# Kernel tuning notes

Hardware: AMD Instinct MI355X
Metric: run time of the kernel (lower is better)

The kernel has to match this reference:

```python
import jax, jax.numpy as jnp
import numpy as np

N = 50000      # nodes
E = 400000     # edges
HID = 128      # hidden size
H = 8          # heads
HS = HID // H  # head size = 16
TN = 8         # node types
R = 8          # relation (edge) types
L = 2          # layers
OUT = 128
EPS = 1e-5
SQRT_D = float(np.sqrt(HS))


def setup_inputs() -> dict:
    key = jax.random.key(0)
    ks = jax.random.split(key, 12)
    s = 1.0 / np.sqrt(HID)
    sh = 1.0 / np.sqrt(HS)
    return {
        "x": jax.random.normal(ks[0], (N, HID), jnp.float32),
        "edge_index": jax.random.randint(ks[1], (2, E), 0, N, dtype=jnp.int32),
        "ntype": jax.random.randint(ks[2], (N,), 0, TN, dtype=jnp.int32),
        "etype": jax.random.randint(ks[3], (E,), 0, R, dtype=jnp.int32),
        "Wk": jax.random.normal(ks[4], (L, TN, HID, HID), jnp.float32) * s,
        "Wq": jax.random.normal(ks[5], (L, TN, HID, HID), jnp.float32) * s,
        "Wv": jax.random.normal(ks[6], (L, TN, HID, HID), jnp.float32) * s,
        "Wa": jax.random.normal(ks[7], (L, TN, HID, HID), jnp.float32) * s,
        "pri": jnp.ones((L, H, R), jnp.float32),
        "Watt": jax.random.normal(ks[8], (L, H, R, HS, HS), jnp.float32) * sh,
        "Wmsg": jax.random.normal(ks[9], (L, H, R, HS, HS), jnp.float32) * sh,
        "skip": jnp.ones((L, TN), jnp.float32),
        "ln_g": jnp.ones((L, HID), jnp.float32),
        "ln_b": jnp.zeros((L, HID), jnp.float32),
        "Wff": jax.random.normal(ks[10], (HID, OUT), jnp.float32) * s,
        "bff": jnp.zeros((OUT,), jnp.float32),
    }


def typed_linear(x, types, W):
    """x:(M,din), types:(M,), W:(T,din,dout) -> (M,dout); y = x @ W[type]."""
    out = jnp.zeros((x.shape[0], W.shape[-1]), x.dtype)
    for t in range(W.shape[0]):
        out = out + jnp.where((types == t)[:, None], x @ W[t], 0.0)
    return out


def rel_apply(h, etype, W):
    """h:(E,H,hs), etype:(E,), W:(H,R,hs,hs) -> (E,H,hs); per-head, per-relation linear."""
    out = jnp.zeros_like(h)
    for r in range(W.shape[1]):
        out = out + jnp.where((etype == r)[:, None, None],
                              jnp.einsum('ehi,hio->eho', h, W[:, r]), 0.0)
    return out


def gt_layer(x, src, dst, ntype, etype, Wk, Wq, Wv, Wa, pri, Watt, Wmsg, skip, g, b):
    n = x.shape[0]
    k = typed_linear(x, ntype, Wk).reshape(n, H, HS)
    q = typed_linear(x, ntype, Wq).reshape(n, H, HS)
    v = typed_linear(x, ntype, Wv).reshape(n, H, HS)
    k_j, q_i, v_j = k[src], q[dst], v[src]          # (E,H,hs)
    kw = rel_apply(k_j, etype, Watt)                # relation-specific key transform
    a = (kw * q_i).sum(-1) * pri[:, etype].T / SQRT_D  # (E,H)
    # scatter softmax over destination nodes
    amax = jax.ops.segment_max(a, dst, num_segments=n)
    ex = jnp.exp(a - amax[dst])
    den = jax.ops.segment_sum(ex, dst, num_segments=n)
    alpha = ex / (den[dst] + 1e-16)
    m = rel_apply(v_j, etype, Wmsg)                 # relation-specific message
    agg = jax.ops.segment_sum(alpha[..., None] * m, dst, num_segments=n)
    out = jax.nn.silu(typed_linear(agg.reshape(n, HID), ntype, Wa))
    al = jax.nn.sigmoid(skip[ntype])[:, None]
    out = out * al + x * (1.0 - al)                 # gated residual (in==hid)
    mu = out.mean(-1, keepdims=True)
    var = ((out - mu) ** 2).mean(-1, keepdims=True)
    return (out - mu) / jnp.sqrt(var + EPS) * g + b


def reference(x, edge_index, ntype, etype, Wk, Wq, Wv, Wa, pri, Watt, Wmsg,
              skip, ln_g, ln_b, Wff, bff):
    src, dst = edge_index[0], edge_index[1]
    emb = x
    for l in range(L):
        emb = gt_layer(emb, src, dst, ntype, etype, Wk[l], Wq[l], Wv[l], Wa[l],
                       pri[l], Watt[l], Wmsg[l], skip[l], ln_g[l], ln_b[l])
    return emb @ Wff + bff
```

## Files before the change

### kernel.cpp

```cpp
#include <hip/hip_runtime.h>
#include <hip/hip_bf16.h>
#include <math.h>

#define N_NODES 50000
#define N_EDGES 400000
#define HID 128
#define NH 8
#define HS 16
#define TN 8
#define NR 8
#define TILE 32
#define MAXTILES 1571
#define PERM_SZ (MAXTILES * TILE)
#define SCAN_BLKS ((N_NODES + 255) / 256)
#define RL_CAP 400128
#define T_GRID 3280

typedef __attribute__((ext_vector_type(8))) short bf16x8;
typedef __attribute__((ext_vector_type(4))) float f32x4;

__device__ __forceinline__ unsigned short f2bf(float f) {
    __hip_bfloat16 h = __float2bfloat16(f);
    return *reinterpret_cast<unsigned short*>(&h);
}
__device__ __forceinline__ float bf2f(unsigned short u) {
    return __uint_as_float((unsigned)u << 16);
}

__global__ void hist_kernel(const int* __restrict__ ntype, int* __restrict__ cnt) {
    __shared__ int l[TN];
    if (threadIdx.x < TN) l[threadIdx.x] = 0;
    __syncthreads();
    int i = blockIdx.x * 256 + threadIdx.x;
    if (i < N_NODES) atomicAdd(&l[ntype[i]], 1);
    __syncthreads();
    if (threadIdx.x < TN) atomicAdd(&cnt[threadIdx.x], l[threadIdx.x]);
}
__global__ void scan_kernel(const int* __restrict__ cnt, int* __restrict__ cursor) {
    if (threadIdx.x == 0 && blockIdx.x == 0) {
        int acc = 0;
        for (int t = 0; t < TN; ++t) {
            cursor[t] = acc;
            acc += ((cnt[t] + TILE - 1) / TILE) * TILE;
        }
    }
}
__global__ void scatter_kernel(const int* __restrict__ ntype, int* __restrict__ cursor,
                               int* __restrict__ perm) {
    __shared__ int lcnt[TN], lbase[TN];
    if (threadIdx.x < TN) lcnt[threadIdx.x] = 0;
    __syncthreads();
    int i = blockIdx.x * 256 + threadIdx.x;
    int t = 0, off = 0;
    if (i < N_NODES) {
        t = ntype[i];
        off = atomicAdd(&lcnt[t], 1);
    }
    __syncthreads();
    if (threadIdx.x < TN)
        lbase[threadIdx.x] = atomicAdd(&cursor[threadIdx.x], lcnt[threadIdx.x]);
    __syncthreads();
    if (i < N_NODES) perm[lbase[t] + off] = i;
}

__global__ void hist_dst_kernel(const int* __restrict__ dst, int* __restrict__ cnt) {
    int e = blockIdx.x * 256 + threadIdx.x;
    if (e < N_EDGES) atomicAdd(&cnt[dst[e]], 1);
}
__global__ void scan_block_kernel(const int* __restrict__ cnt, int* __restrict__ excl,
                                  int* __restrict__ bsum) {
    __shared__ int s[256];
    int tid = threadIdx.x;
    int i = blockIdx.x * 256 + tid;
    int v = (i < N_NODES) ? cnt[i] : 0;
    s[tid] = v;
    __syncthreads();
    for (int off = 1; off < 256; off <<= 1) {
        int t = (tid >= off) ? s[tid - off] : 0;
        __syncthreads();
        s[tid] += t;
        __syncthreads();
    }
    if (i < N_NODES) excl[i] = s[tid] - v;
    if (tid == 255) bsum[blockIdx.x] = s[255];
}
__global__ void scan_top_kernel(int* __restrict__ bsum) {
    __shared__ int s[256];
    int tid = threadIdx.x;
    int v = (tid < SCAN_BLKS) ? bsum[tid] : 0;
    s[tid] = v;
    __syncthreads();
    for (int off = 1; off < 256; off <<= 1) {
        int t = (tid >= off) ? s[tid - off] : 0;
        __syncthreads();
        s[tid] += t;
        __syncthreads();
    }
    if (tid < SCAN_BLKS) bsum[tid] = s[tid] - v;
}
__global__ void scan_add_kernel(int* __restrict__ excl, const int* __restrict__ bsum,
                                int* __restrict__ cursor) {
    int i = blockIdx.x * 256 + threadIdx.x;
    if (i < N_NODES) {
        int v = excl[i] + bsum[blockIdx.x];
        excl[i] = v;
        cursor[i] = v;
    }
}
__global__ void csr_scatter_kernel(const int* __restrict__ src, const int* __restrict__ dst,
                                   const int* __restrict__ etype, int* __restrict__ cur_dst,
                                   int* __restrict__ csr_sd, int* __restrict__ csr_et) {
    int e = blockIdx.x * 256 + threadIdx.x;
    if (e < N_EDGES) {
        int p = atomicAdd(&cur_dst[dst[e]], 1);
        csr_sd[p] = src[e] | (dst[e] << 16);
        csr_et[p] = etype[e];
    }
}

__global__ void ehist_kernel(const int* __restrict__ etype, int* __restrict__ ecnt) {
    __shared__ int l[NR];
    if (threadIdx.x < NR) l[threadIdx.x] = 0;
    __syncthreads();
    int e = blockIdx.x * 256 + threadIdx.x;
    if (e < N_EDGES) atomicAdd(&l[etype[e]], 1);
    __syncthreads();
    if (threadIdx.x < NR) atomicAdd(&ecnt[threadIdx.x], l[threadIdx.x]);
}
__global__ void escan_kernel(const int* __restrict__ ecnt, int* __restrict__ rbase,
                             int* __restrict__ rcur) {
    if (threadIdx.x == 0 && blockIdx.x == 0) {
        int acc = 0;
        for (int r = 0; r < NR; ++r) {
            rbase[r] = acc; rcur[r] = acc;
            acc += ((ecnt[r] + 15) / 16) * 16;
        }
        rbase[NR] = acc;
    }
}
__global__ void rinit_kernel(int* __restrict__ rsd, int* __restrict__ rpos) {
    int i = blockIdx.x * 256 + threadIdx.x;
    if (i < RL_CAP) { rsd[i] = 0; rpos[i] = N_EDGES; }
}
__global__ void rel_scatter_kernel(const int* __restrict__ csr_sd, const int* __restrict__ csr_et,
                                   int* __restrict__ rcur, int* __restrict__ rsd,
                                   int* __restrict__ rpos) {
    __shared__ int lcnt[NR], lbase[NR];
    if (threadIdx.x < NR) lcnt[threadIdx.x] = 0;
    __syncthreads();
    int p = blockIdx.x * 256 + threadIdx.x;
    int r = 0, off = 0;
    if (p < N_EDGES) {
        r = csr_et[p];
        off = atomicAdd(&lcnt[r], 1);
    }
    __syncthreads();
    if (threadIdx.x < NR) lbase[threadIdx.x] = atomicAdd(&rcur[threadIdx.x], lcnt[threadIdx.x]);
    __syncthreads();
    if (p < N_EDGES) {
        int rp = lbase[r] + off;
        rsd[rp] = csr_sd[p];
        rpos[rp] = p;
    }
}

__global__ void wconv_kernel(const float* __restrict__ W, unsigned short* __restrict__ out) {
    int mat = blockIdx.x >> 3, seg = blockIdx.x & 7;
    const float* w = W + (size_t)mat * HID * HID;
    unsigned short* o = out + (size_t)mat * HID * HID;
#pragma unroll
    for (int c = 0; c < 8; ++c) {
        int idx = seg * 2048 + c * 256 + threadIdx.x;
        int i = idx >> 7, j = idx & 127;
        o[j * HID + i] = f2bf(w[idx]);
    }
}
__global__ void wsmall_conv(const float* __restrict__ W, const float* __restrict__ pri,
                            unsigned short* __restrict__ out) {
    int blk = blockIdx.x;
    int tid = threadIdx.x;
    int i = tid >> 4, o = tid & 15;
    float s = pri ? pri[blk] * 0.25f : 1.f;
    out[blk * 256 + o * 16 + i] = f2bf(W[blk * 256 + i * 16 + o] * s);
}

__global__ __launch_bounds__(256) void gemm3_mfma(
    const float* __restrict__ x, const int* __restrict__ perm, const int* __restrict__ ntype,
    const unsigned short* __restrict__ WkT, const unsigned short* __restrict__ WqT,
    const unsigned short* __restrict__ WvT,
    unsigned short* __restrict__ Kb, unsigned short* __restrict__ Qb,
    unsigned short* __restrict__ Vb) {
    __shared__ unsigned short xs[TILE][HID + 8];
    __shared__ int nodes[TILE];
    int tid = threadIdx.x;
    if (tid < TILE) nodes[tid] = perm[blockIdx.x * TILE + tid];
    __syncthreads();
    if (nodes[0] < 0) return;
    int t = ntype[nodes[0]];
#pragma unroll
    for (int c = 0; c < 4; ++c) {
        int v = tid + c * 256;
        int ns = v >> 5, ii = (v & 31) * 4;
        int node = nodes[ns];
        float4 val = (node >= 0) ? *(const float4*)(x + (size_t)node * HID + ii)
                                 : make_float4(0.f, 0.f, 0.f, 0.f);
        uint2 pk;
        pk.x = (unsigned)f2bf(val.x) | ((unsigned)f2bf(val.y) << 16);
        pk.y = (unsigned)f2bf(val.z) | ((unsigned)f2bf(val.w) << 16);
        *(uint2*)&xs[ns][ii] = pk;
    }
    __syncthreads();
    int wv = tid >> 6, lane = tid & 63;
    int lrow = lane & 15, lk = lane >> 4;
    bf16x8 af[2][4];
#pragma unroll
    for (int rt = 0; rt < 2; ++rt)
#pragma unroll
        for (int kk = 0; kk < 4; ++kk)
            af[rt][kk] = *(const bf16x8*)&xs[rt * 16 + lrow][kk * 32 + lk * 8];
    size_t woff = (size_t)t * HID * HID + (size_t)lrow * HID + lk * 8;
#pragma unroll
    for (int pp = 0; pp < 6; ++pp) {
        int p = wv * 6 + pp;
        int mat = p >> 3, ct = p & 7;
        const unsigned short* wb =
            (mat == 0 ? WkT : (mat == 1 ? WqT : WvT)) + woff + (size_t)ct * 16 * HID;
        unsigned short* ob = (mat == 0) ? Kb : (mat == 1 ? Qb : Vb);
        f32x4 a0 = {0.f, 0.f, 0.f, 0.f}, a1 = {0.f, 0.f, 0.f, 0.f};
#pragma unroll
        for (int kk = 0; kk < 4; ++kk) {
            bf16x8 bfr = *(const bf16x8*)(wb + kk * 32);
            a0 = __builtin_amdgcn_mfma_f32_16x16x32_bf16(af[0][kk], bfr, a0, 0, 0, 0);
            a1 = __builtin_amdgcn_mfma_f32_16x16x32_bf16(af[1][kk], bfr, a1, 0, 0, 0);
        }
        int col = ct * 16 + lrow;
#pragma unroll
        for (int q = 0; q < 4; ++q) {
            int r0 = lk * 4 + q;
            int n0 = nodes[r0], n1 = nodes[16 + r0];
            if (n0 >= 0) ob[(size_t)n0 * HID + col] = f2bf(a0[q]);
            if (n1 >= 0) ob[(size_t)n1 * HID + col] = f2bf(a1[q]);
        }
    }
}

__global__ __launch_bounds__(256) void gemm1_mfma(
    const float* __restrict__ x, const int* __restrict__ perm, const int* __restrict__ ntype,
    const unsigned short* __restrict__ Wt, const float* __restrict__ bias,
    float* __restrict__ out) {
    __shared__ unsigned short xs[TILE][HID + 8];
    __shared__ int nodes[TILE];
    int tid = threadIdx.x;
    if (tid < TILE) {
        int n;
        if (perm) n = perm[blockIdx.x * TILE + tid];
        else { n = blockIdx.x * TILE + tid; if (n >= N_NODES) n = -1; }
        nodes[tid] = n;
    }
    __syncthreads();
    if (nodes[0] < 0) return;
    int t = perm ? ntype[nodes[0]] : 0;
#pragma unroll
    for (int c = 0; c < 4; ++c) {
        int v = tid + c * 256;
        int ns = v >> 5, ii = (v & 31) * 4;
        int node = nodes[ns];
        float4 val = (node >= 0) ? *(const float4*)(x + (size_t)node * HID + ii)
                                 : make_float4(0.f, 0.f, 0.f, 0.f);
        uint2 pk;
        pk.x = (unsigned)f2bf(val.x) | ((unsigned)f2bf(val.y) << 16);
        pk.y = (unsigned)f2bf(val.z) | ((unsigned)f2bf(val.w) << 16);
        *(uint2*)&xs[ns][ii] = pk;
    }
    __syncthreads();
    int wv = tid >> 6, lane = tid & 63;
    int lrow = lane & 15, lk = lane >> 4;
    bf16x8 af[2][4];
#pragma unroll
    for (int rt = 0; rt < 2; ++rt)
#pragma unroll
        for (int kk = 0; kk < 4; ++kk)
            af[rt][kk] = *(const bf16x8*)&xs[rt * 16 + lrow][kk * 32 + lk * 8];
    const unsigned short* wb0 = Wt + (size_t)t * HID * HID + (size_t)lrow * HID + lk * 8;
#pragma unroll
    for (int pp = 0; pp < 2; ++pp) {
        int ct = wv * 2 + pp;
        const unsigned short* wb = wb0 + (size_t)ct * 16 * HID;
        f32x4 a0 = {0.f, 0.f, 0.f, 0.f}, a1 = {0.f, 0.f, 0.f, 0.f};
#pragma unroll
        for (int kk = 0; kk < 4; ++kk) {
            bf16x8 bfr = *(const bf16x8*)(wb + kk * 32);
            a0 = __builtin_amdgcn_mfma_f32_16x16x32_bf16(af[0][kk], bfr, a0, 0, 0, 0);
            a1 = __builtin_amdgcn_mfma_f32_16x16x32_bf16(af[1][kk], bfr, a1, 0, 0, 0);
        }
        float bv = bias ? bias[ct * 16 + lrow] : 0.f;
#pragma unroll
        for (int q = 0; q < 4; ++q) {
            int r0 = lk * 4 + q;
            int n0 = nodes[r0], n1 = nodes[16 + r0];
            if (n0 >= 0) out[(size_t)n0 * HID + ct * 16 + lrow] = a0[q] + bv;
            if (n1 >= 0) out[(size_t)n1 * HID + ct * 16 + lrow] = a1[q] + bv;
        }
    }
}

__global__ __launch_bounds__(256) void gemm1_ln_mfma(
    const unsigned short* __restrict__ aggb, const int* __restrict__ perm,
    const int* __restrict__ ntype, const unsigned short* __restrict__ Wt,
    const float* __restrict__ xin, const float* __restrict__ skip,
    const float* __restrict__ g, const float* __restrict__ b, float* __restrict__ xout) {
    __shared__ unsigned short xs[TILE][HID + 8];
    __shared__ int nodes[TILE];
    __shared__ float psum[TILE][4], psq[TILE][4];
    __shared__ float mu_s[TILE], rv_s[TILE];
    int tid = threadIdx.x;
    if (tid < TILE) nodes[tid] = perm[blockIdx.x * TILE + tid];
    __syncthreads();
    if (nodes[0] < 0) return;
    int t = ntype[nodes[0]];
#pragma unroll
    for (int c = 0; c < 4; ++c) {
        int v = tid + c * 256;
        int ns = v >> 5, ii = (v & 31) * 4;
        int node = nodes[ns];
        uint2 pk = make_uint2(0u, 0u);
        if (node >= 0) pk = *(const uint2*)(aggb + (size_t)node * HID + ii);
        *(uint2*)&xs[ns][ii] = pk;
    }
    __syncthreads();
    int wv = tid >> 6, lane = tid & 63;
    int lrow = lane & 15, lk = lane >> 4;
    bf16x8 af[2][4];
#pragma unroll
    for (int rt = 0; rt < 2; ++rt)
#pragma unroll
        for (int kk = 0; kk < 4; ++kk)
            af[rt][kk] = *(const bf16x8*)&xs[rt * 16 + lrow][kk * 32 + lk * 8];
    const unsigned short* wb0 = Wt + (size_t)t * HID * HID + (size_t)lrow * HID + lk * 8;
    float al = 1.f / (1.f + __expf(-skip[t]));
    float om = 1.f - al;
    float ov[2][2][4];
#pragma unroll
    for (int pp = 0; pp < 2; ++pp) {
        int ct = wv * 2 + pp;
        const unsigned short* wb = wb0 + (size_t)ct * 16 * HID;
        f32x4 a0 = {0.f, 0.f, 0.f, 0.f}, a1 = {0.f, 0.f, 0.f, 0.f};
#pragma unroll
        for (int kk = 0; kk < 4; ++kk) {
            bf16x8 bfr = *(const bf16x8*)(wb + kk * 32);
            a0 = __builtin_amdgcn_mfma_f32_16x16x32_bf16(af[0][kk], bfr, a0, 0, 0, 0);
            a1 = __builtin_amdgcn_mfma_f32_16x16x32_bf16(af[1][kk], bfr, a1, 0, 0, 0);
        }
        int col = ct * 16 + lrow;
#pragma unroll
        for (int q = 0; q < 4; ++q) {
            int n0 = nodes[lk * 4 + q], n1 = nodes[16 + lk * 4 + q];
            float s0 = a0[q] / (1.f + __expf(-a0[q]));
            float s1 = a1[q] / (1.f + __expf(-a1[q]));
            float x0 = (n0 >= 0) ? xin[(size_t)n0 * HID + col] : 0.f;
            float x1 = (n1 >= 0) ? xin[(size_t)n1 * HID + col] : 0.f;
            ov[pp][0][q] = s0 * al + x0 * om;
            ov[pp][1][q] = s1 * al + x1 * om;
        }
    }
#pragma unroll
    for (int half = 0; half < 2; ++half)
#pragma unroll
        for (int q = 0; q < 4; ++q) {
            float s = ov[0][half][q] + ov[1][half][q];
            float s2 = ov[0][half][q] * ov[0][half][q] + ov[1][half][q] * ov[1][half][q];
            s += __shfl_xor(s, 1); s += __shfl_xor(s, 2);
            s += __shfl_xor(s, 4); s += __shfl_xor(s, 8);
            s2 += __shfl_xor(s2, 1); s2 += __shfl_xor(s2, 2);
            s2 += __shfl_xor(s2, 4); s2 += __shfl_xor(s2, 8);
            if (lrow == 0) {
                int nd = half * 16 + lk * 4 + q;
                psum[nd][wv] = s;
                psq[nd][wv] = s2;
            }
        }
    __syncthreads();
    if (tid < TILE) {
        float s = psum[tid][0] + psum[tid][1] + psum[tid][2] + psum[tid][3];
        float s2 = psq[tid][0] + psq[tid][1] + psq[tid][2] + psq[tid][3];
        float mu = s * (1.f / HID);
        float var = s2 * (1.f / HID) - mu * mu;
        mu_s[tid] = mu;
        rv_s[tid] = rsqrtf(fmaxf(var, 0.f) + 1e-5f);
    }
    __syncthreads();
#pragma unroll
    for (int pp = 0; pp < 2; ++pp) {
        int col = (wv * 2 + pp) * 16 + lrow;
        float gg = g[col], bb = b[col];
#pragma unroll
        for (int q = 0; q < 4; ++q) {
            int i0 = lk * 4 + q, i1 = 16 + lk * 4 + q;
            int n0 = nodes[i0], n1 = nodes[i1];
            if (n0 >= 0) xout[(size_t)n0 * HID + col] = (ov[pp][0][q] - mu_s[i0]) * rv_s[i0] * gg + bb;
            if (n1 >= 0) xout[(size_t)n1 * HID + col] = (ov[pp][1][q] - mu_s[i1]) * rv_s[i1] * gg + bb;
        }
    }
}

__global__ __launch_bounds__(512) void transform_kernel(
    const unsigned short* __restrict__ Kb, const unsigned short* __restrict__ Vb,
    const unsigned short* __restrict__ Qb,
    const int* __restrict__ rsd, const int* __restrict__ rpos, const int* __restrict__ rbase,
    const unsigned short* __restrict__ WattT, const unsigned short* __restrict__ WmsgT,
    float* __restrict__ scores, unsigned short* __restrict__ mg) {
    __shared__ unsigned short smg[8][16][136];
    __shared__ float ssc[8][16][8];
    int wv = threadIdx.x >> 6;
    int r = wv;
    int lane = threadIdx.x & 63;
    int ecol = lane & 15, lk = lane >> 4;
    int tbeg = rbase[r] + blockIdx.x * 16;
    if (tbeg >= rbase[r + 1]) return;
    int entry = tbeg + ecol;
    int sd = rsd[entry];
    int s = sd & 0xFFFF, dd = (sd >> 16) & 0xFFFF;
    int p = rpos[entry];

    const bf16x8 zz = {0, 0, 0, 0, 0, 0, 0, 0};
#pragma unroll
    for (int h = 0; h < NH; ++h) {
        bf16x8 bk = zz, bv = zz, aa = zz, am = zz;
        if (lk < 2) {
            bk = *(const bf16x8*)(Kb + (size_t)s * HID + h * HS + lk * 8);
            bv = *(const bf16x8*)(Vb + (size_t)s * HID + h * HS + lk * 8);
            int wo = ((h * NR + r) * 16 + ecol) * 16 + lk * 8;
            aa = *(const bf16x8*)(WattT + wo);
            am = *(const bf16x8*)(WmsgT + wo);
        }
        f32x4 ck = {0.f, 0.f, 0.f, 0.f}, cm = {0.f, 0.f, 0.f, 0.f};
        ck = __builtin_amdgcn_mfma_f32_16x16x32_bf16(aa, bk, ck, 0, 0, 0);
        cm = __builtin_amdgcn_mfma_f32_16x16x32_bf16(am, bv, cm, 0, 0, 0);
        uint2 qraw = *(const uint2*)(Qb + (size_t)dd * HID + h * HS + lk * 4);
        float q0 = __uint_as_float(qraw.x << 16);
        float q1 = __uint_as_float(qraw.x & 0xffff0000u);
        float q2 = __uint_as_float(qraw.y << 16);
        float q3 = __uint_as_float(qraw.y & 0xffff0000u);
        float xsc = ck[0] * q0 + ck[1] * q1 + ck[2] * q2 + ck[3] * q3;
        xsc += __shfl_xor(xsc, 16);
        xsc += __shfl_xor(xsc, 32);
        if (lk == 0) ssc[wv][ecol][h] = xsc;
        uint2 pk2;
        pk2.x = (unsigned)f2bf(cm[0]) | ((unsigned)f2bf(cm[1]) << 16);
        pk2.y = (unsigned)f2bf(cm[2]) | ((unsigned)f2bf(cm[3]) << 16);
        *(uint2*)&smg[wv][ecol][h * 16 + lk * 4] = pk2;
    }
    int gq = lane >> 3, sub = lane & 7;
#pragma unroll
    for (int c = 0; c < 4; ++c) {
        int li = c * 8 + gq;
        int e = li >> 1, half = li & 1;
        int pe = __shfl(p, e);
        uint4 v = *(const uint4*)&smg[wv][e][half * 64 + sub * 8];
        *(uint4*)(mg + (size_t)pe * HID + half * 64 + sub * 8) = v;
    }
    int es = lane >> 1;
    int pe2 = __shfl(p, es & 15);
    if (lane < 32) {
        int hh = lane & 1;
        float4 v = *(const float4*)&ssc[wv][es][hh * 4];
        *(float4*)(scores + (size_t)pe2 * NH + hh * 4) = v;
    }
}

__global__ __launch_bounds__(256) void edge_soft_kernel(
    const float* __restrict__ scores, const unsigned short* __restrict__ mg,
    const int* __restrict__ row_ptr, const int* __restrict__ deg,
    unsigned short* __restrict__ aggb) {
    int d = blockIdx.x * 4 + (threadIdx.x >> 6);
    if (d >= N_NODES) return;
    int lane = threadIdx.x & 63;
    int h = lane >> 3, j = lane & 7;
    int beg = row_ptr[d], dg = deg[d];

    const float* sc = scores + (size_t)beg * NH + h;
    const unsigned short* mgp = mg + (size_t)beg * HID + h * HS + j * 2;

    float m = -INFINITY, den = 0.f, a0 = 0.f, a1 = 0.f;
    for (int e = 0; e < dg; ++e) {
        float a = sc[(size_t)e * NH];
        unsigned mgu = *(const unsigned*)(mgp + (size_t)e * HID);
        float g0 = __uint_as_float(mgu << 16);
        float g1 = __uint_as_float(mgu & 0xffff0000u);
        float mn = fmaxf(m, a);
        float scale = __expf(m - mn);
        float ex = __expf(a - mn);
        den = den * scale + ex;
        a0 = a0 * scale + ex * g0;
        a1 = a1 * scale + ex * g1;
        m = mn;
    }
    float inv = 1.f / (den + 1e-16f);
    unsigned r0 = (unsigned)f2bf(a0 * inv);
    unsigned r1 = (unsigned)f2bf(a1 * inv);
    *(unsigned*)(aggb + (size_t)d * HID + h * HS + j * 2) = r0 | (r1 << 16);
}

extern "C" void kernel_launch(void* const* d_in, const int* in_sizes, int n_in,
                              void* d_out, int out_size, void* d_ws, size_t ws_size,
                              hipStream_t stream) {
    const float* x     = (const float*)d_in[0];
    const int*   eidx  = (const int*)d_in[1];
    const int*   ntype = (const int*)d_in[2];
    const int*   etype = (const int*)d_in[3];
    const float* Wk    = (const float*)d_in[4];
    const float* Wq    = (const float*)d_in[5];
    const float* Wv    = (const float*)d_in[6];
    const float* Wa    = (const float*)d_in[7];
    const float* pri   = (const float*)d_in[8];
    const float* Watt  = (const float*)d_in[9];
    const float* Wmsg  = (const float*)d_in[10];
    const float* skip  = (const float*)d_in[11];
    const float* ln_g  = (const float*)d_in[12];
    const float* ln_b  = (const float*)d_in[13];
    const float* Wff   = (const float*)d_in[14];
    const float* bff   = (const float*)d_in[15];
    const int* src = eidx;
    const int* dst = eidx + N_EDGES;

    char* ws = (char*)d_ws;
    size_t szN = (size_t)N_NODES * HID * sizeof(float);
    float* embA = (float*)(ws);
    unsigned short* AGGb = (unsigned short*)(ws + szN);
    char*  kvq  = ws + 2 * szN;
    unsigned short* Kbf = (unsigned short*)kvq;
    unsigned short* Vbf = (unsigned short*)(kvq + (size_t)N_NODES * HID * 2);
    unsigned short* Qbf = (unsigned short*)(kvq + 2 * (size_t)N_NODES * HID * 2);
    float* l1out = (float*)kvq;
    char*  p    = kvq + 3 * (size_t)N_NODES * HID * 2;
    int* perm    = (int*)p;  p += (size_t)PERM_SZ * 4;
    int* cnt     = (int*)p;  p += TN * 4;
    int* cursor  = (int*)p;  p += TN * 4;
    int* row_ptr = (int*)p;  p += (size_t)N_NODES * 4;
    int* cnt_dst = (int*)p;  p += (size_t)N_NODES * 4;
    int* cur_dst = (int*)p;  p += (size_t)N_NODES * 4;
    int* bsum    = (int*)p;  p += 256 * 4;
    int* ecnt    = (int*)p;  p += NR * 4;
    int* rbase   = (int*)p;  p += (NR + 1) * 4;
    int* rcur    = (int*)p;  p += NR * 4;
    int* csr_sd  = (int*)p;  p += (size_t)N_EDGES * 4;
    int* csr_et  = (int*)p;  p += (size_t)N_EDGES * 4;
    int* rsd     = (int*)p;  p += (size_t)RL_CAP * 4;
    int* rpos    = (int*)p;  p += (size_t)RL_CAP * 4;
    size_t wmat = (size_t)HID * HID;
    unsigned short* WkT  = (unsigned short*)p;  p += 2 * TN * wmat * 2;
    unsigned short* WqT  = (unsigned short*)p;  p += 2 * TN * wmat * 2;
    unsigned short* WvT  = (unsigned short*)p;  p += 2 * TN * wmat * 2;
    unsigned short* WaT  = (unsigned short*)p;  p += 2 * TN * wmat * 2;
    unsigned short* WffT = (unsigned short*)p;  p += wmat * 2;
    unsigned short* WattT = (unsigned short*)p; p += 2 * 64 * 256 * 2;
    unsigned short* WmsgT = (unsigned short*)p; p += 2 * 64 * 256 * 2;
    p = (char*)(((size_t)p + 255) & ~(size_t)255);
    float* scores = (float*)p;          p += (size_t)(N_EDGES + 16) * NH * 4;
    unsigned short* mg = (unsigned short*)p;  p += (size_t)(N_EDGES + 16) * HID * 2;

    wconv_kernel<<<2 * TN * 8, 256, 0, stream>>>(Wk, WkT);
    wconv_kernel<<<2 * TN * 8, 256, 0, stream>>>(Wq, WqT);
    wconv_kernel<<<2 * TN * 8, 256, 0, stream>>>(Wv, WvT);
    wconv_kernel<<<2 * TN * 8, 256, 0, stream>>>(Wa, WaT);
    wconv_kernel<<<8, 256, 0, stream>>>(Wff, WffT);
    wsmall_conv<<<128, 256, 0, stream>>>(Watt, pri, WattT);
    wsmall_conv<<<128, 256, 0, stream>>>(Wmsg, nullptr, WmsgT);

    hipMemsetAsync(cnt, 0, TN * 4, stream);
    hipMemsetAsync(perm, 0xFF, (size_t)PERM_SZ * 4, stream);
    hist_kernel<<<(N_NODES + 255) / 256, 256, 0, stream>>>(ntype, cnt);
    scan_kernel<<<1, 64, 0, stream>>>(cnt, cursor);
    scatter_kernel<<<(N_NODES + 255) / 256, 256, 0, stream>>>(ntype, cursor, perm);

    hipMemsetAsync(cnt_dst, 0, (size_t)N_NODES * 4, stream);
    hipMemsetAsync(ecnt, 0, NR * 4, stream);
    hist_dst_kernel<<<(N_EDGES + 255) / 256, 256, 0, stream>>>(dst, cnt_dst);
    ehist_kernel<<<(N_EDGES + 255) / 256, 256, 0, stream>>>(etype, ecnt);
    scan_block_kernel<<<SCAN_BLKS, 256, 0, stream>>>(cnt_dst, row_ptr, bsum);
    scan_top_kernel<<<1, 256, 0, stream>>>(bsum);
    scan_add_kernel<<<SCAN_BLKS, 256, 0, stream>>>(row_ptr, bsum, cur_dst);
    csr_scatter_kernel<<<(N_EDGES + 255) / 256, 256, 0, stream>>>(src, dst, etype, cur_dst,
                                                                  csr_sd, csr_et);
    escan_kernel<<<1, 64, 0, stream>>>(ecnt, rbase, rcur);
    rinit_kernel<<<(RL_CAP + 255) / 256, 256, 0, stream>>>(rsd, rpos);
    rel_scatter_kernel<<<(N_EDGES + 255) / 256, 256, 0, stream>>>(csr_sd, csr_et, rcur,
                                                                  rsd, rpos);

    for (int l = 0; l < 2; ++l) {
        const float* xin = l ? embA : x;
        float* xout = l ? l1out : embA;
        const float* skip_l = skip + (size_t)l * TN;
        const float* g_l    = ln_g + (size_t)l * HID;
        const float* b_l    = ln_b + (size_t)l * HID;
        const unsigned short* WkT_l = WkT + (size_t)l * TN * wmat;
        const unsigned short* WqT_l = WqT + (size_t)l * TN * wmat;
        const unsigned short* WvT_l = WvT + (size_t)l * TN * wmat;
        const unsigned short* WaT_l = WaT + (size_t)l * TN * wmat;
        const unsigned short* WattT_l = WattT + (size_t)l * 64 * 256;
        const unsigned short* WmsgT_l = WmsgT + (size_t)l * 64 * 256;

        gemm3_mfma<<<MAXTILES, 256, 0, stream>>>(xin, perm, ntype, WkT_l, WqT_l, WvT_l,
                                                 Kbf, Qbf, Vbf);
        transform_kernel<<<T_GRID, 512, 0, stream>>>(Kbf, Vbf, Qbf, rsd, rpos, rbase,
                                                     WattT_l, WmsgT_l, scores, mg);
        edge_soft_kernel<<<(N_NODES + 3) / 4, 256, 0, stream>>>(scores, mg, row_ptr, cnt_dst,
                                                                AGGb);
        gemm1_ln_mfma<<<MAXTILES, 256, 0, stream>>>(AGGb, perm, ntype, WaT_l, xin,
                                                    skip_l, g_l, b_l, xout);
    }
    gemm1_mfma<<<(N_NODES + TILE - 1) / TILE, 256, 0, stream>>>(l1out, nullptr, ntype, WffT,
                                                                bff, (float*)d_out);
}
```

Before: 488.4 us.

## Fuse relation transform and segment softmax per destination-node block in LDS

Replaces the global relation-sorted edge lists with per-block relation tiles covering 16 destination nodes, built by a new btile_build kernel. A single fused kernel computes the relation-specific attention scores and messages with MFMA into shared memory, then does the online softmax aggregation directly from LDS. This removes the global round-trip of the per-edge scores and bf16 messages and one kernel launch per layer. In exchange it pads each relation to whole 16-edge tiles per block, which wastes some MFMA work, and it runs the heads in two passes. It also relies on fixed caps (288 edges and 26 tiles per block) that hold for these random inputs but are not guaranteed for arbitrary graphs.

```diff
diff --git a/kernel.cpp b/kernel.cpp
--- a/kernel.cpp
+++ b/kernel.cpp
@@ -13,8 +13,9 @@
 #define MAXTILES 1571
 #define PERM_SZ (MAXTILES * TILE)
 #define SCAN_BLKS ((N_NODES + 255) / 256)
-#define RL_CAP 400128
-#define T_GRID 3280
+#define NB 3125
+#define TPBMAX 26
+#define CAP 288
 
 typedef __attribute__((ext_vector_type(8))) short bf16x8;
 typedef __attribute__((ext_vector_type(4))) float f32x4;
@@ -118,49 +119,43 @@
     }
 }
 
-__global__ void ehist_kernel(const int* __restrict__ etype, int* __restrict__ ecnt) {
-    __shared__ int l[NR];
-    if (threadIdx.x < NR) l[threadIdx.x] = 0;
-    __syncthreads();
-    int e = blockIdx.x * 256 + threadIdx.x;
-    if (e < N_EDGES) atomicAdd(&l[etype[e]], 1);
-    __syncthreads();
-    if (threadIdx.x < NR) atomicAdd(&ecnt[threadIdx.x], l[threadIdx.x]);
-}
-__global__ void escan_kernel(const int* __restrict__ ecnt, int* __restrict__ rbase,
-                             int* __restrict__ rcur) {
-    if (threadIdx.x == 0 && blockIdx.x == 0) {
-        int acc = 0;
-        for (int r = 0; r < NR; ++r) {
-            rbase[r] = acc; rcur[r] = acc;
-            acc += ((ecnt[r] + 15) / 16) * 16;
-        }
-        rbase[NR] = acc;
-    }
-}
-__global__ void rinit_kernel(int* __restrict__ rsd, int* __restrict__ rpos) {
-    int i = blockIdx.x * 256 + threadIdx.x;
-    if (i < RL_CAP) { rsd[i] = 0; rpos[i] = N_EDGES; }
-}
-__global__ void rel_scatter_kernel(const int* __restrict__ csr_sd, const int* __restrict__ csr_et,
-                                   int* __restrict__ rcur, int* __restrict__ rsd,
-                                   int* __restrict__ rpos) {
-    __shared__ int lcnt[NR], lbase[NR];
-    if (threadIdx.x < NR) lcnt[threadIdx.x] = 0;
-    __syncthreads();
-    int p = blockIdx.x * 256 + threadIdx.x;
-    int r = 0, off = 0;
-    if (p < N_EDGES) {
-        r = csr_et[p];
-        off = atomicAdd(&lcnt[r], 1);
-    }
-    __syncthreads();
-    if (threadIdx.x < NR) lbase[threadIdx.x] = atomicAdd(&rcur[threadIdx.x], lcnt[threadIdx.x]);
-    __syncthreads();
-    if (p < N_EDGES) {
-        int rp = lbase[r] + off;
-        rsd[rp] = csr_sd[p];
-        rpos[rp] = p;
+__global__ void btile_build(const int* __restrict__ row_ptr,
+                            const int* __restrict__ csr_sd, const int* __restrict__ csr_et,
+                            int* __restrict__ btile_sd, int* __restrict__ btile_lp,
+                            int* __restrict__ btile_r, int* __restrict__ ntb) {
+    int b = blockIdx.x;
+    int lane = threadIdx.x;
+    int p0 = row_ptr[b * 16];
+    int p1 = (b == NB - 1) ? N_EDGES : row_ptr[b * 16 + 16];
+    int cnt = 0;
+    if (lane < 8) {
+        for (int p = p0; p < p1; ++p) cnt += (csr_et[p] == lane);
+    }
+    int tiles = (cnt + 15) >> 4;
+    int pre = 0, total = 0;
+    for (int k = 0; k < 8; ++k) {
+        int tk = __shfl(tiles, k);
+        if (k < lane) pre += tk;
+        total += tk;
+    }
+    if (lane == 0) ntb[b] = total;
+    if (lane < 8) {
+        int tbase = b * TPBMAX + pre;
+        for (int t = 0; t < tiles; ++t) btile_r[tbase + t] = lane;
+        int off = 0;
+        for (int p = p0; p < p1; ++p) {
+            if (csr_et[p] == lane) {
+                int idx = (tbase + (off >> 4)) * 16 + (off & 15);
+                btile_sd[idx] = csr_sd[p];
+                btile_lp[idx] = p - p0;
+                ++off;
+            }
+        }
+        for (; off < tiles * 16; ++off) {
+            int idx = (tbase + (off >> 4)) * 16 + (off & 15);
+            btile_sd[idx] = 0;
+            btile_lp[idx] = CAP;
+        }
     }
 }
 
@@ -403,102 +398,84 @@
     }
 }
 
-__global__ __launch_bounds__(512) void transform_kernel(
+__global__ __launch_bounds__(512) void fused_attn_kernel(
     const unsigned short* __restrict__ Kb, const unsigned short* __restrict__ Vb,
     const unsigned short* __restrict__ Qb,
-    const int* __restrict__ rsd, const int* __restrict__ rpos, const int* __restrict__ rbase,
+    const int* __restrict__ row_ptr, const int* __restrict__ deg,
+    const int* __restrict__ btile_sd, const int* __restrict__ btile_lp,
+    const int* __restrict__ btile_r, const int* __restrict__ ntb,
     const unsigned short* __restrict__ WattT, const unsigned short* __restrict__ WmsgT,
-    float* __restrict__ scores, unsigned short* __restrict__ mg) {
-    __shared__ unsigned short smg[8][16][136];
-    __shared__ float ssc[8][16][8];
-    int wv = threadIdx.x >> 6;
-    int r = wv;
-    int lane = threadIdx.x & 63;
+    unsigned short* __restrict__ aggb) {
+    __shared__ unsigned short smg[CAP + 1][72];
+    __shared__ float ssc[CAP + 1][4];
+    int b = blockIdx.x;
+    int wv = threadIdx.x >> 6, lane = threadIdx.x & 63;
     int ecol = lane & 15, lk = lane >> 4;
-    int tbeg = rbase[r] + blockIdx.x * 16;
-    if (tbeg >= rbase[r + 1]) return;
-    int entry = tbeg + ecol;
-    int sd = rsd[entry];
-    int s = sd & 0xFFFF, dd = (sd >> 16) & 0xFFFF;
-    int p = rpos[entry];
-
+    int nt = ntb[b];
+    int p0 = row_ptr[b * 16];
     const bf16x8 zz = {0, 0, 0, 0, 0, 0, 0, 0};
-#pragma unroll
-    for (int h = 0; h < NH; ++h) {
-        bf16x8 bk = zz, bv = zz, aa = zz, am = zz;
-        if (lk < 2) {
-            bk = *(const bf16x8*)(Kb + (size_t)s * HID + h * HS + lk * 8);
-            bv = *(const bf16x8*)(Vb + (size_t)s * HID + h * HS + lk * 8);
-            int wo = ((h * NR + r) * 16 + ecol) * 16 + lk * 8;
-            aa = *(const bf16x8*)(WattT + wo);
-            am = *(const bf16x8*)(WmsgT + wo);
-        }
-        f32x4 ck = {0.f, 0.f, 0.f, 0.f}, cm = {0.f, 0.f, 0.f, 0.f};
-        ck = __builtin_amdgcn_mfma_f32_16x16x32_bf16(aa, bk, ck, 0, 0, 0);
-        cm = __builtin_amdgcn_mfma_f32_16x16x32_bf16(am, bv, cm, 0, 0, 0);
-        uint2 qraw = *(const uint2*)(Qb + (size_t)dd * HID + h * HS + lk * 4);
-        float q0 = __uint_as_float(qraw.x << 16);
-        float q1 = __uint_as_float(qraw.x & 0xffff0000u);
-        float q2 = __uint_as_float(qraw.y << 16);
-        float q3 = __uint_as_float(qraw.y & 0xffff0000u);
-        float xsc = ck[0] * q0 + ck[1] * q1 + ck[2] * q2 + ck[3] * q3;
-        xsc += __shfl_xor(xsc, 16);
-        xsc += __shfl_xor(xsc, 32);
-        if (lk == 0) ssc[wv][ecol][h] = xsc;
-        uint2 pk2;
-        pk2.x = (unsigned)f2bf(cm[0]) | ((unsigned)f2bf(cm[1]) << 16);
-        pk2.y = (unsigned)f2bf(cm[2]) | ((unsigned)f2bf(cm[3]) << 16);
-        *(uint2*)&smg[wv][ecol][h * 16 + lk * 4] = pk2;
-    }
-    int gq = lane >> 3, sub = lane & 7;
-#pragma unroll
-    for (int c = 0; c < 4; ++c) {
-        int li = c * 8 + gq;
-        int e = li >> 1, half = li & 1;
-        int pe = __shfl(p, e);
-        uint4 v = *(const uint4*)&smg[wv][e][half * 64 + sub * 8];
-        *(uint4*)(mg + (size_t)pe * HID + half * 64 + sub * 8) = v;
-    }
-    int es = lane >> 1;
-    int pe2 = __shfl(p, es & 15);
-    if (lane < 32) {
-        int hh = lane & 1;
-        float4 v = *(const float4*)&ssc[wv][es][hh * 4];
-        *(float4*)(scores + (size_t)pe2 * NH + hh * 4) = v;
-    }
-}
-
-__global__ __launch_bounds__(256) void edge_soft_kernel(
-    const float* __restrict__ scores, const unsigned short* __restrict__ mg,
-    const int* __restrict__ row_ptr, const int* __restrict__ deg,
-    unsigned short* __restrict__ aggb) {
-    int d = blockIdx.x * 4 + (threadIdx.x >> 6);
-    if (d >= N_NODES) return;
-    int lane = threadIdx.x & 63;
-    int h = lane >> 3, j = lane & 7;
-    int beg = row_ptr[d], dg = deg[d];
-
-    const float* sc = scores + (size_t)beg * NH + h;
-    const unsigned short* mgp = mg + (size_t)beg * HID + h * HS + j * 2;
-
-    float m = -INFINITY, den = 0.f, a0 = 0.f, a1 = 0.f;
-    for (int e = 0; e < dg; ++e) {
-        float a = sc[(size_t)e * NH];
-        unsigned mgu = *(const unsigned*)(mgp + (size_t)e * HID);
-        float g0 = __uint_as_float(mgu << 16);
-        float g1 = __uint_as_float(mgu & 0xffff0000u);
-        float mn = fmaxf(m, a);
-        float scale = __expf(m - mn);
-        float ex = __expf(a - mn);
-        den = den * scale + ex;
-        a0 = a0 * scale + ex * g0;
-        a1 = a1 * scale + ex * g1;
-        m = mn;
-    }
-    float inv = 1.f / (den + 1e-16f);
-    unsigned r0 = (unsigned)f2bf(a0 * inv);
-    unsigned r1 = (unsigned)f2bf(a1 * inv);
-    *(unsigned*)(aggb + (size_t)d * HID + h * HS + j * 2) = r0 | (r1 << 16);
+
+#pragma unroll
+    for (int pass = 0; pass < 2; ++pass) {
+        int hbase = pass * 4;
+        for (int t = wv; t < nt; t += 8) {
+            int ti = b * TPBMAX + t;
+            int r = btile_r[ti];
+            int sd = btile_sd[ti * 16 + ecol];
+            int lp = btile_lp[ti * 16 + ecol];
+            int s = sd & 0xFFFF, dd = ((unsigned)sd >> 16);
+#pragma unroll
+            for (int hh = 0; hh < 4; ++hh) {
+                int h = hbase + hh;
+                bf16x8 bk = zz, bv = zz, aa = zz, am = zz;
+                if (lk < 2) {
+                    bk = *(const bf16x8*)(Kb + (size_t)s * HID + h * HS + lk * 8);
+                    bv = *(const bf16x8*)(Vb + (size_t)s * HID + h * HS + lk * 8);
+                    int wo = ((h * NR + r) * 16 + ecol) * 16 + lk * 8;
+                    aa = *(const bf16x8*)(WattT + wo);
+                    am = *(const bf16x8*)(WmsgT + wo);
+                }
+                f32x4 ck = {0.f, 0.f, 0.f, 0.f}, cm = {0.f, 0.f, 0.f, 0.f};
+                ck = __builtin_amdgcn_mfma_f32_16x16x32_bf16(aa, bk, ck, 0, 0, 0);
+                cm = __builtin_amdgcn_mfma_f32_16x16x32_bf16(am, bv, cm, 0, 0, 0);
+                uint2 qraw = *(const uint2*)(Qb + (size_t)dd * HID + h * HS + lk * 4);
+                float q0 = __uint_as_float(qraw.x << 16);
+                float q1 = __uint_as_float(qraw.x & 0xffff0000u);
+                float q2 = __uint_as_float(qraw.y << 16);
+                float q3 = __uint_as_float(qraw.y & 0xffff0000u);
+                float xsc = ck[0] * q0 + ck[1] * q1 + ck[2] * q2 + ck[3] * q3;
+                xsc += __shfl_xor(xsc, 16);
+                xsc += __shfl_xor(xsc, 32);
+                if (lk == 0) ssc[lp][hh] = xsc;
+                uint2 pk2;
+                pk2.x = (unsigned)f2bf(cm[0]) | ((unsigned)f2bf(cm[1]) << 16);
+                pk2.y = (unsigned)f2bf(cm[2]) | ((unsigned)f2bf(cm[3]) << 16);
+                *(uint2*)&smg[lp][hh * 16 + lk * 4] = pk2;
+            }
+        }
+        __syncthreads();
+        int h2 = lane >> 4, o = lane & 15;
+#pragma unroll
+        for (int i = 0; i < 2; ++i) {
+            int d = b * 16 + wv * 2 + i;
+            int lo = row_ptr[d] - p0;
+            int dg = deg[d];
+            float m = -INFINITY, den = 0.f, acc = 0.f;
+            for (int e = 0; e < dg; ++e) {
+                int lp = lo + e;
+                float a = ssc[lp][h2];
+                float gv = bf2f(smg[lp][h2 * 16 + o]);
+                float mn = fmaxf(m, a);
+                float scale = __expf(m - mn);
+                float ex = __expf(a - mn);
+                den = den * scale + ex;
+                acc = acc * scale + ex * gv;
+                m = mn;
+            }
+            aggb[(size_t)d * HID + (hbase + h2) * HS + o] = f2bf(acc / (den + 1e-16f));
+        }
+        __syncthreads();
+    }
 }
 
 extern "C" void kernel_launch(void* const* d_in, const int* in_sizes, int n_in,
@@ -540,13 +517,12 @@
     int* cnt_dst = (int*)p;  p += (size_t)N_NODES * 4;
     int* cur_dst = (int*)p;  p += (size_t)N_NODES * 4;
     int* bsum    = (int*)p;  p += 256 * 4;
-    int* ecnt    = (int*)p;  p += NR * 4;
-    int* rbase   = (int*)p;  p += (NR + 1) * 4;
-    int* rcur    = (int*)p;  p += NR * 4;
     int* csr_sd  = (int*)p;  p += (size_t)N_EDGES * 4;
     int* csr_et  = (int*)p;  p += (size_t)N_EDGES * 4;
-    int* rsd     = (int*)p;  p += (size_t)RL_CAP * 4;
-    int* rpos    = (int*)p;  p += (size_t)RL_CAP * 4;
+    int* btile_sd = (int*)p; p += (size_t)NB * TPBMAX * 16 * 4;
+    int* btile_lp = (int*)p; p += (size_t)NB * TPBMAX * 16 * 4;
+    int* btile_r  = (int*)p; p += (size_t)NB * TPBMAX * 4;
+    int* ntb      = (int*)p; p += (size_t)NB * 4;
     size_t wmat = (size_t)HID * HID;
     unsigned short* WkT  = (unsigned short*)p;  p += 2 * TN * wmat * 2;
     unsigned short* WqT  = (unsigned short*)p;  p += 2 * TN * wmat * 2;
@@ -555,9 +531,6 @@
     unsigned short* WffT = (unsigned short*)p;  p += wmat * 2;
     unsigned short* WattT = (unsigned short*)p; p += 2 * 64 * 256 * 2;
     unsigned short* WmsgT = (unsigned short*)p; p += 2 * 64 * 256 * 2;
-    p = (char*)(((size_t)p + 255) & ~(size_t)255);
-    float* scores = (float*)p;          p += (size_t)(N_EDGES + 16) * NH * 4;
-    unsigned short* mg = (unsigned short*)p;  p += (size_t)(N_EDGES + 16) * HID * 2;
 
     wconv_kernel<<<2 * TN * 8, 256, 0, stream>>>(Wk, WkT);
     wconv_kernel<<<2 * TN * 8, 256, 0, stream>>>(Wq, WqT);
@@ -574,18 +547,14 @@
     scatter_kernel<<<(N_NODES + 255) / 256, 256, 0, stream>>>(ntype, cursor, perm);
 
     hipMemsetAsync(cnt_dst, 0, (size_t)N_NODES * 4, stream);
-    hipMemsetAsync(ecnt, 0, NR * 4, stream);
     hist_dst_kernel<<<(N_EDGES + 255) / 256, 256, 0, stream>>>(dst, cnt_dst);
-    ehist_kernel<<<(N_EDGES + 255) / 256, 256, 0, stream>>>(etype, ecnt);
     scan_block_kernel<<<SCAN_BLKS, 256, 0, stream>>>(cnt_dst, row_ptr, bsum);
     scan_top_kernel<<<1, 256, 0, stream>>>(bsum);
     scan_add_kernel<<<SCAN_BLKS, 256, 0, stream>>>(row_ptr, bsum, cur_dst);
     csr_scatter_kernel<<<(N_EDGES + 255) / 256, 256, 0, stream>>>(src, dst, etype, cur_dst,
                                                                   csr_sd, csr_et);
-    escan_kernel<<<1, 64, 0, stream>>>(ecnt, rbase, rcur);
-    rinit_kernel<<<(RL_CAP + 255) / 256, 256, 0, stream>>>(rsd, rpos);
-    rel_scatter_kernel<<<(N_EDGES + 255) / 256, 256, 0, stream>>>(csr_sd, csr_et, rcur,
-                                                                  rsd, rpos);
+    btile_build<<<NB, 64, 0, stream>>>(row_ptr, csr_sd, csr_et,
+                                       btile_sd, btile_lp, btile_r, ntb);
 
     for (int l = 0; l < 2; ++l) {
         const float* xin = l ? embA : x;
@@ -602,10 +571,9 @@
 
         gemm3_mfma<<<MAXTILES, 256, 0, stream>>>(xin, perm, ntype, WkT_l, WqT_l, WvT_l,
                                                  Kbf, Qbf, Vbf);
-        transform_kernel<<<T_GRID, 512, 0, stream>>>(Kbf, Vbf, Qbf, rsd, rpos, rbase,
-                                                     WattT_l, WmsgT_l, scores, mg);
-        edge_soft_kernel<<<(N_NODES + 3) / 4, 256, 0, stream>>>(scores, mg, row_ptr, cnt_dst,
-                                                                AGGb);
+        fused_attn_kernel<<<NB, 512, 0, stream>>>(Kbf, Vbf, Qbf, row_ptr, cnt_dst,
+                                                  btile_sd, btile_lp, btile_r, ntb,
+                                                  WattT_l, WmsgT_l, AGGb);
         gemm1_ln_mfma<<<MAXTILES, 256, 0, stream>>>(AGGb, perm, ntype, WaT_l, xin,
                                                     skip_l, g_l, b_l, xout);
     }
```

Result: faster. 438.8 us (-10.2%).
